# Optimization experiments

Measured on AMD Instinct MI355X. Metric: run time of the kernel, lower is better.

Reference implementation:

```python
import jax, jax.numpy as jnp
import numpy as np

H = 1000   # hidden_size
B = 64     # batch
S = 512    # encoder source length


def setup_inputs() -> dict:
    key = jax.random.key(0)
    ks = jax.random.split(key, 9)
    scale = 0.02
    return {
        "decoder_hidden": jax.random.normal(ks[0], (1, B, H), jnp.float32),
        "context": jax.random.normal(ks[1], (B, S, 2 * H), jnp.float32),
        "mask": jax.random.randint(ks[2], (B, S, 1), 0, 2) == 1,
        "W_a": jax.random.normal(ks[3], (H, 2 * H), jnp.float32) * scale,
        "W_b": jax.random.normal(ks[4], (H, H), jnp.float32) * scale,
        "W_c_w": jax.random.normal(ks[5], (1, H), jnp.float32) * scale,
        "W_c_b": jax.random.normal(ks[6], (1,), jnp.float32) * scale,
        "dense_w": jax.random.normal(ks[7], (H, 2 * H), jnp.float32) * scale,
        "dense_b": jax.random.normal(ks[8], (H,), jnp.float32) * scale,
    }


def reference(decoder_hidden, context, mask, W_a, W_b, W_c_w, W_c_b, dense_w, dense_b):
    # context_in: (B, S, H)
    context_in = jnp.einsum('bsd,hd->bsh', context, W_a)
    # hidden_in: (1, B, H) @ W_b.T -> transpose(0,1) -> (B, 1, H)
    hidden_in = jnp.transpose(jnp.einsum('nbd,hd->nbh', decoder_hidden, W_b), (1, 0, 2))
    # scores: (B, S, 1)
    attention = jnp.einsum('bsh,oh->bso', jnp.tanh(context_in + hidden_in), W_c_w) + W_c_b
    attention = jnp.where(mask, jnp.asarray(-1e6, attention.dtype), attention)
    attention_softmaxed = jax.nn.softmax(attention, axis=1)  # softmax over source length
    # weighted_sum: (B, 1, S) x (B, S, 2H) -> (B, 1, 2H)
    weighted_sum = jnp.einsum('bso,bsd->bod', attention_softmaxed, context)
    # dense: (B, 1, H)
    return jnp.einsum('bod,hd->boh', weighted_sum, dense_w) + dense_b
```

## Files before the change

### kernel.cpp

```cpp
#include <hip/hip_runtime.h>
#include <hip/hip_bf16.h>

#define H 1000
#define B 64
#define S 512
#define D 2000
#define KP 2048
#define NP 1024
#define MP 32768
#define KS 10

typedef __attribute__((ext_vector_type(8))) short short8;
typedef __attribute__((ext_vector_type(4))) float f32x4;
typedef __attribute__((ext_vector_type(16))) float f32x16;

__device__ inline unsigned short f2bf(float f) {
  __hip_bfloat16 h = __float2bfloat16(f);
  union { __hip_bfloat16 h; unsigned short u; } c; c.h = h;
  return c.u;
}
__device__ inline float bf2f(unsigned short u) {
  union { unsigned u; float f; } x; x.u = ((unsigned)u) << 16;
  return x.f;
}
__device__ inline float tanh_fast(float x) {
  float e2 = __expf(2.f * x);
  return 1.f - 2.f / (e2 + 1.f);
}

__global__ __launch_bounds__(256) void k_dect(const float* __restrict__ dec,
                                              float* __restrict__ dec_t) {
  const int d = blockIdx.x * 4 + (threadIdx.x >> 6);
  const int b = threadIdx.x & 63;
  dec_t[d * 64 + b] = dec[b * H + d];
}

__global__ __launch_bounds__(256) void k_hidden2(const float* __restrict__ dec_t,
                                                 const float* __restrict__ Wb,
                                                 float* __restrict__ hi) {
  const int h = blockIdx.x * 4 + (threadIdx.x >> 6);
  const int lane = threadIdx.x & 63;
  const float* w = Wb + (size_t)h * H;
  float acc = 0.f;
#pragma unroll 4
  for (int d = 0; d < H; ++d) acc += w[d] * dec_t[d * 64 + lane];
  hi[lane * H + h] = acc;
}

__global__ __launch_bounds__(256) void k_hidden(const float* __restrict__ dec,
                                                const float* __restrict__ Wb,
                                                float* __restrict__ hi) {
  __shared__ float sdec[H];
  const int b = blockIdx.y;
  const int h = blockIdx.x * 4 + (threadIdx.x >> 6);
  const int lane = threadIdx.x & 63;
  for (int d = threadIdx.x; d < H; d += 256) sdec[d] = dec[b * H + d];
  __syncthreads();
  const float* w = Wb + (size_t)h * H;
  float acc = 0.f;
  for (int d = lane; d < H; d += 64) acc += w[d] * sdec[d];
  for (int o = 32; o; o >>= 1) acc += __shfl_xor(acc, o);
  if (lane == 0) hi[b * H + h] = acc;
}

__global__ __launch_bounds__(256) void k_cvt_t(const float* __restrict__ src,
                                               unsigned short* __restrict__ dst,
                                               int valid_rows) {
  __shared__ unsigned short st[2][8192];
  const int rp = blockIdx.x;
  const int tid = threadIdx.x;
  const int r0 = tid >> 2;
  const int kq = tid & 3;

#define CVT_BODY(T, P)                                                          \
  do {                                                                          \
    const int t = (T);                                                          \
    unsigned short v[4][8];                                                     \
    _Pragma("unroll")                                                           \
    for (int w = 0; w < 4; ++w) {                                               \
      const int grow = rp * 256 + r0 + w * 64;                                  \
      const int gcol = t * 32 + kq * 8;                                         \
      if (grow < valid_rows && gcol + 8 <= D) {                                 \
        const float* p = src + (size_t)grow * D + gcol;                         \
        float4 x = *(const float4*)p;                                           \
        float4 y = *(const float4*)(p + 4);                                     \
        v[w][0] = f2bf(x.x); v[w][1] = f2bf(x.y); v[w][2] = f2bf(x.z);          \
        v[w][3] = f2bf(x.w); v[w][4] = f2bf(y.x); v[w][5] = f2bf(y.y);          \
        v[w][6] = f2bf(y.z); v[w][7] = f2bf(y.w);                               \
      } else {                                                                  \
        _Pragma("unroll")                                                       \
        for (int z = 0; z < 8; ++z) v[w][z] = 0;                                \
      }                                                                         \
    }                                                                           \
    _Pragma("unroll")                                                           \
    for (int w = 0; w < 4; ++w)                                                 \
      *(short8*)&st[P][(kq * 256 + r0 + w * 64) * 8] = *(short8*)&v[w][0];      \
    __syncthreads();                                                            \
    unsigned short* ob = dst + ((size_t)rp * 64 + t) * 8192;                    \
    _Pragma("unroll")                                                           \
    for (int s = 0; s < 4; ++s)                                                 \
      *(short8*)(ob + (tid + s * 256) * 8) = *(short8*)&st[P][(tid + s * 256) * 8]; \
  } while (0)

  const int t0 = blockIdx.y * 8;
  for (int tt = 0; tt < 8; tt += 2) {
    CVT_BODY(t0 + tt, 0);
    CVT_BODY(t0 + tt + 1, 1);
  }
#undef CVT_BODY
}

__global__ __launch_bounds__(512) void k_scores_fast(const unsigned short* __restrict__ ctxb,
                                                     const unsigned short* __restrict__ wab,
                                                     const float* __restrict__ hi,
                                                     const float* __restrict__ Wcw,
                                                     float* __restrict__ scores) {
  __shared__ unsigned short As[3][8192];
  __shared__ unsigned short Bs[3][8192];

  const int bid = blockIdx.x;
  const int swz = (bid & 7) * 64 + (bid >> 3);
  const int rtile = swz >> 2;
  const int ctile = swz & 3;
  const int row0 = rtile * 256;
  const int col0 = ctile * 256;

  const int tid = threadIdx.x;
  const int lane = tid & 63;
  const int wid = tid >> 6;
  const int wm = wid >> 2;
  const int wn = wid & 3;
  const int ln31 = lane & 31;
  const int kh = lane >> 5;

  const unsigned short* ga = ctxb + (size_t)rtile * (64 * 8192);
  const unsigned short* gb = wab + (size_t)ctile * (64 * 8192);

  f32x16 acc[4][2];
#pragma unroll
  for (int i = 0; i < 4; ++i)
#pragma unroll
    for (int j = 0; j < 2; ++j)
#pragma unroll
      for (int r = 0; r < 16; ++r) acc[i][j][r] = 0.f;

#define STAGE(T, BUF)                                                                                      \
  do {                                                                                                     \
    const unsigned short* pa = ga + (size_t)(T) * 8192 + tid * 8;                                          \
    const unsigned short* pb = gb + (size_t)(T) * 8192 + tid * 8;                                          \
    __builtin_amdgcn_global_load_lds((const __attribute__((address_space(1))) unsigned int*)pa,            \
                                     (__attribute__((address_space(3))) unsigned int*)&As[BUF][tid * 8],   \
                                     16, 0, 0);                                                            \
    __builtin_amdgcn_global_load_lds((const __attribute__((address_space(1))) unsigned int*)(pa + 4096),   \
                                     (__attribute__((address_space(3))) unsigned int*)&As[BUF][tid * 8 + 4096], \
                                     16, 0, 0);                                                            \
    __builtin_amdgcn_global_load_lds((const __attribute__((address_space(1))) unsigned int*)pb,            \
                                     (__attribute__((address_space(3))) unsigned int*)&Bs[BUF][tid * 8],   \
                                     16, 0, 0);                                                            \
    __builtin_amdgcn_global_load_lds((const __attribute__((address_space(1))) unsigned int*)(pb + 4096),   \
                                     (__attribute__((address_space(3))) unsigned int*)&Bs[BUF][tid * 8 + 4096], \
                                     16, 0, 0);                                                            \
  } while (0)

  const int abase = kh * 2048 + (wm * 128 + ln31) * 8;
  const int bbase = kh * 2048 + (wn * 64 + ln31) * 8;

#define COMPUTE(BI)                                                                     \
  do {                                                                                  \
    _Pragma("unroll")                                                                   \
    for (int ks = 0; ks < 2; ++ks) {                                                    \
      short8 a[4], bb[2];                                                               \
      _Pragma("unroll")                                                                 \
      for (int mi = 0; mi < 4; ++mi)                                                    \
        a[mi] = *(const short8*)&As[BI][abase + ks * 4096 + mi * 256];                  \
      _Pragma("unroll")                                                                 \
      for (int ni = 0; ni < 2; ++ni)                                                    \
        bb[ni] = *(const short8*)&Bs[BI][bbase + ks * 4096 + ni * 256];                 \
      __builtin_amdgcn_s_setprio(1);                                                    \
      _Pragma("unroll")                                                                 \
      for (int mi = 0; mi < 4; ++mi)                                                    \
        _Pragma("unroll")                                                               \
        for (int ni = 0; ni < 2; ++ni)                                                  \
          acc[mi][ni] = __builtin_amdgcn_mfma_f32_32x32x16_bf16(a[mi], bb[ni], acc[mi][ni], 0, 0, 0); \
      __builtin_amdgcn_s_setprio(0);                                                    \
    }                                                                                   \
  } while (0)

#define ITER(T, BC, BS)                                      \
  do {                                                       \
    STAGE((T) + 2, BS);                                      \
    COMPUTE(BC);                                             \
    asm volatile("s_waitcnt vmcnt(4)" ::: "memory");         \
    __builtin_amdgcn_s_barrier();                            \
  } while (0)

  STAGE(0, 0);
  STAGE(1, 1);
  asm volatile("s_waitcnt vmcnt(4)" ::: "memory");
  __builtin_amdgcn_s_barrier();

  for (int t = 0; t < 60; t += 3) {
    ITER(t, 0, 2);
    ITER(t + 1, 1, 0);
    ITER(t + 2, 2, 1);
  }
  ITER(60, 0, 2);
  ITER(61, 1, 0);
  COMPUTE(2);
  asm volatile("s_waitcnt vmcnt(0)" ::: "memory");
  __builtin_amdgcn_s_barrier();
  COMPUTE(0);
#undef ITER
#undef STAGE
#undef COMPUTE

  const int b_idx = row0 >> 9;
  float wc[2], hv[2];
#pragma unroll
  for (int ni = 0; ni < 2; ++ni) {
    const int h = col0 + wn * 64 + ni * 32 + ln31;
    wc[ni] = (h < H) ? Wcw[h] : 0.f;
    hv[ni] = (h < H) ? hi[b_idx * H + h] : 0.f;
  }
#pragma unroll
  for (int mi = 0; mi < 4; ++mi) {
#pragma unroll
    for (int reg = 0; reg < 16; ++reg) {
      float p = wc[0] * tanh_fast(acc[mi][0][reg] + hv[0])
              + wc[1] * tanh_fast(acc[mi][1][reg] + hv[1]);
      p += __shfl_xor(p, 1);
      p += __shfl_xor(p, 2);
      p += __shfl_xor(p, 4);
      p += __shfl_xor(p, 8);
      p += __shfl_xor(p, 16);
      if (ln31 == 0) {
        const int n = row0 + wm * 128 + mi * 32 + (reg & 3) + 8 * (reg >> 2) + 4 * kh;
        atomicAdd(&scores[n], p);
      }
    }
  }
}

#define BM 128
#define BN 128
#define BK 32
#define NT 63
__global__ __launch_bounds__(256) void k_scores(const float* __restrict__ ctx,
                                                const float* __restrict__ Wa,
                                                const float* __restrict__ hi,
                                                const float* __restrict__ Wcw,
                                                float* __restrict__ scores) {
  __shared__ unsigned short As[2][BM][BK];
  __shared__ unsigned short Bs[2][BN][BK];

  const int bid = blockIdx.x;
  const int swz = (bid & 7) * 256 + (bid >> 3);
  const int row0 = (swz >> 3) * BM;
  const int col0 = (swz & 7) * BN;

  const int tid = threadIdx.x;
  const int lane = tid & 63;
  const int wid = tid >> 6;
  const int wm = wid >> 1;
  const int wn = wid & 1;
  const int fr = lane & 15;
  const int fq = lane >> 4;

  const int trow = tid >> 1;
  const int thalf = tid & 1;

  f32x4 acc[4][4];
#pragma unroll
  for (int i = 0; i < 4; ++i)
#pragma unroll
    for (int j = 0; j < 4; ++j) acc[i][j] = (f32x4){0.f, 0.f, 0.f, 0.f};

  const float* aptr = ctx + (size_t)(row0 + trow) * D + thalf * 16;
  const int hB = col0 + trow;
  const bool bvalid = (hB < H);
  const float* bptr = Wa + (size_t)(bvalid ? hB : 0) * D + thalf * 16;

  float4 ra[4], rb[4];

#define LOADT(T)                                                     \
  do {                                                               \
    const int base = (T) * BK + thalf * 16;                          \
    _Pragma("unroll")                                                \
    for (int q = 0; q < 4; ++q) {                                    \
      const int kk = base + q * 4;                                   \
      if (kk < D) {                                                  \
        ra[q] = *(const float4*)(aptr + (T) * BK + q * 4);           \
        if (bvalid) rb[q] = *(const float4*)(bptr + (T) * BK + q * 4); \
      }                                                              \
    }                                                                \
  } while (0)

#define CVTW(T, BUF)                                                 \
  do {                                                               \
    const int base = (T) * BK + thalf * 16;                          \
    unsigned short ta[16], tb[16];                                   \
    _Pragma("unroll")                                                \
    for (int q = 0; q < 4; ++q) {                                    \
      const int kk = base + q * 4;                                   \
      const bool v = (kk < D);                                       \
      ta[q * 4 + 0] = v ? f2bf(ra[q].x) : 0;                         \
      ta[q * 4 + 1] = v ? f2bf(ra[q].y) : 0;                         \
      ta[q * 4 + 2] = v ? f2bf(ra[q].z) : 0;                         \
      ta[q * 4 + 3] = v ? f2bf(ra[q].w) : 0;                         \
      const bool vb = v && bvalid;                                   \
      tb[q * 4 + 0] = vb ? f2bf(rb[q].x) : 0;                        \
      tb[q * 4 + 1] = vb ? f2bf(rb[q].y) : 0;                        \
      tb[q * 4 + 2] = vb ? f2bf(rb[q].z) : 0;                        \
      tb[q * 4 + 3] = vb ? f2bf(rb[q].w) : 0;                        \
    }                                                                \
    *(short8*)&As[BUF][trow][thalf * 16]     = *(short8*)&ta[0];     \
    *(short8*)&As[BUF][trow][thalf * 16 + 8] = *(short8*)&ta[8];     \
    *(short8*)&Bs[BUF][trow][thalf * 16]     = *(short8*)&tb[0];     \
    *(short8*)&Bs[BUF][trow][thalf * 16 + 8] = *(short8*)&tb[8];     \
  } while (0)

  LOADT(0);
  CVTW(0, 0);
  LOADT(1);
  __syncthreads();

  int cur = 0;
  for (int t = 0; t < NT; ++t) {
    short8 a[4], bbf[4];
#pragma unroll
    for (int mi = 0; mi < 4; ++mi)
      a[mi] = *(const short8*)&As[cur][wm * 64 + mi * 16 + fr][fq * 8];
#pragma unroll
    for (int ni = 0; ni < 4; ++ni)
      bbf[ni] = *(const short8*)&Bs[cur][wn * 64 + ni * 16 + fr][fq * 8];
#pragma unroll
    for (int mi = 0; mi < 4; ++mi)
#pragma unroll
      for (int ni = 0; ni < 4; ++ni)
        acc[mi][ni] = __builtin_amdgcn_mfma_f32_16x16x32_bf16(a[mi], bbf[ni], acc[mi][ni], 0, 0, 0);

    if (t + 1 < NT) {
      CVTW(t + 1, cur ^ 1);
      if (t + 2 < NT) LOADT(t + 2);
    }
    __syncthreads();
    cur ^= 1;
  }
#undef LOADT
#undef CVTW

  const int b_idx = row0 >> 9;
  float wcv[4], hiv[4];
#pragma unroll
  for (int ni = 0; ni < 4; ++ni) {
    const int h = col0 + wn * 64 + ni * 16 + fr;
    wcv[ni] = (h < H) ? Wcw[h] : 0.f;
    hiv[ni] = (h < H) ? hi[b_idx * H + h] : 0.f;
  }
#pragma unroll
  for (int mi = 0; mi < 4; ++mi) {
#pragma unroll
    for (int r = 0; r < 4; ++r) {
      float p = 0.f;
#pragma unroll
      for (int ni = 0; ni < 4; ++ni)
        p += wcv[ni] * tanhf(acc[mi][ni][r] + hiv[ni]);
      p += __shfl_xor(p, 1);
      p += __shfl_xor(p, 2);
      p += __shfl_xor(p, 4);
      p += __shfl_xor(p, 8);
      if (fr == 0)
        atomicAdd(&scores[row0 + wm * 64 + mi * 16 + fq * 4 + r], p);
    }
  }
}

__global__ __launch_bounds__(256) void k_softmax(const float* __restrict__ scores,
                                                 const int* __restrict__ mask,
                                                 const float* __restrict__ Wcb,
                                                 float* __restrict__ probs) {
  __shared__ float buf[S];
  __shared__ float rbuf[256];
  const int b = blockIdx.x;
  const float bias = Wcb[0];
  float mx = -3.4e38f;
  for (int s = threadIdx.x; s < S; s += 256) {
    float a = mask[b * S + s] ? -1e6f : (scores[b * S + s] + bias);
    buf[s] = a;
    mx = fmaxf(mx, a);
  }
  rbuf[threadIdx.x] = mx;
  __syncthreads();
  for (int w = 128; w > 0; w >>= 1) {
    if (threadIdx.x < w) rbuf[threadIdx.x] = fmaxf(rbuf[threadIdx.x], rbuf[threadIdx.x + w]);
    __syncthreads();
  }
  mx = rbuf[0];
  __syncthreads();
  float sum = 0.f;
  for (int s = threadIdx.x; s < S; s += 256) {
    float e = expf(buf[s] - mx);
    buf[s] = e;
    sum += e;
  }
  rbuf[threadIdx.x] = sum;
  __syncthreads();
  for (int w = 128; w > 0; w >>= 1) {
    if (threadIdx.x < w) rbuf[threadIdx.x] += rbuf[threadIdx.x + w];
    __syncthreads();
  }
  const float inv = 1.f / rbuf[0];
  for (int s = threadIdx.x; s < S; s += 256) probs[b * S + s] = buf[s] * inv;
}

__global__ __launch_bounds__(256) void k_wsum_b(const unsigned short* __restrict__ ctxb,
                                                const float* __restrict__ probs,
                                                float* __restrict__ ws2) {
  __shared__ float sp[S];
  const int t = blockIdx.x;
  const int b = blockIdx.y;
  const int tid = threadIdx.x;
  const int p = tid >> 6;
  const int lane = tid & 63;
  for (int i = tid; i < S; i += 256) sp[i] = probs[b * S + i];
  __syncthreads();
  float acc[8];
#pragma unroll
  for (int e = 0; e < 8; ++e) acc[e] = 0.f;
#pragma unroll
  for (int rt = 0; rt < 2; ++rt) {
    const unsigned short* chunk = ctxb + ((size_t)(b * 2 + rt) * 64 + t) * 8192;
#pragma unroll
    for (int half = 0; half < 4; ++half) {
      const int row = half * 64 + lane;
      short8 v = *(const short8*)&chunk[(p * 256 + row) * 8];
      const float pv = sp[rt * 256 + row];
#pragma unroll
      for (int e = 0; e < 8; ++e) acc[e] += pv * bf2f((unsigned short)v[e]);
    }
  }
#pragma unroll
  for (int o = 32; o; o >>= 1)
#pragma unroll
    for (int e = 0; e < 8; ++e) acc[e] += __shfl_xor(acc[e], o);
  const int d0 = t * 32 + p * 8;
  if (lane == 0 && d0 < D) {
#pragma unroll
    for (int e = 0; e < 8; ++e) ws2[(size_t)b * D + d0 + e] = acc[e];
  }
}

__global__ __launch_bounds__(256) void k_wsum(const float* __restrict__ ctx,
                                              const float* __restrict__ probs,
                                              float* __restrict__ ws2) {
  __shared__ float p[S];
  const int b = blockIdx.y;
  const int d = blockIdx.x * 256 + threadIdx.x;
  for (int s = threadIdx.x; s < S; s += 256) p[s] = probs[b * S + s];
  __syncthreads();
  if (d < D) {
    float acc = 0.f;
    for (int s = 0; s < S; ++s) acc += p[s] * ctx[(size_t)(b * S + s) * D + d];
    ws2[b * D + d] = acc;
  }
}

__global__ __launch_bounds__(256) void k_dense_part(const float* __restrict__ ws2,
                                                    const float* __restrict__ Dw,
                                                    float* __restrict__ partial) {
  __shared__ float sw[64][201];
  const int tid = threadIdx.x;
  const int ks = blockIdx.y;
  const int k0 = ks * 200;
  for (int idx = tid; idx < 64 * 200; idx += 256) {
    const int b = idx / 200, k = idx - b * 200;
    sw[b][k] = ws2[(size_t)b * D + k0 + k];
  }
  __syncthreads();
  const int h = blockIdx.x * 4 + (tid >> 6);
  const int lane = tid & 63;
  const float* wrow = Dw + (size_t)h * D + k0;
  float acc = 0.f;
#pragma unroll 8
  for (int k = 0; k < 200; ++k) acc += wrow[k] * sw[lane][k];
  partial[((size_t)ks * 64 + lane) * 1000 + h] = acc;
}

__global__ __launch_bounds__(256) void k_dense_red(const float* __restrict__ partial,
                                                   const float* __restrict__ Db,
                                                   float* __restrict__ out) {
  const int idx = blockIdx.x * 256 + threadIdx.x;
  const int h = idx % 1000;
  float acc = Db[h];
#pragma unroll
  for (int ks = 0; ks < KS; ++ks) acc += partial[(size_t)ks * 64000 + idx];
  out[idx] = acc;
}

__global__ __launch_bounds__(256) void k_dense(const float* __restrict__ ws2,
                                               const float* __restrict__ Dw,
                                               const float* __restrict__ Db,
                                               float* __restrict__ out) {
  __shared__ float v[D];
  const int b = blockIdx.y;
  const int h = blockIdx.x * 256 + threadIdx.x;
  for (int d = threadIdx.x; d < D; d += 256) v[d] = ws2[b * D + d];
  __syncthreads();
  if (h < H) {
    const float* w = Dw + (size_t)h * D;
    float acc = 0.f;
    for (int d = 0; d < D; ++d) acc += w[d] * v[d];
    out[b * H + h] = acc + Db[h];
  }
}

extern "C" void kernel_launch(void* const* d_in, const int* in_sizes, int n_in,
                              void* d_out, int out_size, void* d_ws, size_t ws_size,
                              hipStream_t stream) {
  const float* dec = (const float*)d_in[0];
  const float* ctx = (const float*)d_in[1];
  const int*   mask = (const int*)d_in[2];
  const float* Wa  = (const float*)d_in[3];
  const float* Wb  = (const float*)d_in[4];
  const float* Wcw = (const float*)d_in[5];
  const float* Wcb = (const float*)d_in[6];
  const float* Dw  = (const float*)d_in[7];
  const float* Db  = (const float*)d_in[8];
  float* out = (float*)d_out;

  float* hi     = (float*)d_ws;
  float* scores = hi + B * H;
  float* probs  = scores + B * S;
  float* ws2    = probs + B * S;
  const size_t float_words = (size_t)B * H + 2 * B * S + B * D;
  unsigned short* ctx_b = (unsigned short*)((float*)d_ws + float_words);
  unsigned short* wa_b  = ctx_b + (size_t)MP * KP;
  float* dec_t  = (float*)ctx_b;
  float* partial = (float*)ctx_b;
  const size_t need = float_words * 4 + ((size_t)MP * KP + (size_t)NP * KP) * 2;

  hipMemsetAsync(scores, 0, B * S * sizeof(float), stream);
  if (ws_size >= need) {
    k_dect<<<250, 256, 0, stream>>>(dec, dec_t);
    k_hidden2<<<250, 256, 0, stream>>>(dec_t, Wb, hi);
    k_cvt_t<<<dim3(MP / 256, 8), 256, 0, stream>>>(ctx, ctx_b, MP);
    k_cvt_t<<<dim3(NP / 256, 8), 256, 0, stream>>>(Wa, wa_b, H);
    k_scores_fast<<<512, 512, 0, stream>>>(ctx_b, wa_b, hi, Wcw, scores);
    k_softmax<<<B, 256, 0, stream>>>(scores, mask, Wcb, probs);
    k_wsum_b<<<dim3(63, B), 256, 0, stream>>>(ctx_b, probs, ws2);
    k_dense_part<<<dim3(250, KS), 256, 0, stream>>>(ws2, Dw, partial);
    k_dense_red<<<250, 256, 0, stream>>>(partial, Db, out);
  } else {
    k_hidden<<<dim3(250, B), 256, 0, stream>>>(dec, Wb, hi);
    k_scores<<<2048, 256, 0, stream>>>(ctx, Wa, hi, Wcw, scores);
    k_softmax<<<B, 256, 0, stream>>>(scores, mask, Wcb, probs);
    k_wsum<<<dim3((D + 255) / 256, B), 256, 0, stream>>>(ctx, probs, ws2);
    k_dense<<<dim3((H + 255) / 256, B), 256, 0, stream>>>(ws2, Dw, Db, out);
  }
}
```

Baseline: 408.5 us.

## Double scores GEMM block threads and fuse softmax into weighted-sum kernel

The scores GEMM now launches 1024 threads per block, 16 waves each owning a 64x64 sub-tile instead of 8 waves with 128x64. Each thread issues half as many LDS-direct loads, and the waitcnt values drop to match. The softmax kernel is removed: every weighted-sum block recomputes the masked softmax for its batch row from the raw scores before accumulating. This cuts a launch and the probs round trip, at the cost of redundant softmax work across 63 blocks per batch row and a possible change in GEMM occupancy and register pressure.

Result: no change. 407.4 us (-0.3%).

```diff
diff --git a/kernel.cpp b/kernel.cpp
--- a/kernel.cpp
+++ b/kernel.cpp
@@ -110,11 +110,11 @@
 #undef CVT_BODY
 }
 
-__global__ __launch_bounds__(512) void k_scores_fast(const unsigned short* __restrict__ ctxb,
-                                                     const unsigned short* __restrict__ wab,
-                                                     const float* __restrict__ hi,
-                                                     const float* __restrict__ Wcw,
-                                                     float* __restrict__ scores) {
+__global__ __launch_bounds__(1024) void k_scores_fast(const unsigned short* __restrict__ ctxb,
+                                                      const unsigned short* __restrict__ wab,
+                                                      const float* __restrict__ hi,
+                                                      const float* __restrict__ Wcw,
+                                                      float* __restrict__ scores) {
   __shared__ unsigned short As[3][8192];
   __shared__ unsigned short Bs[3][8192];
 
@@ -136,9 +136,9 @@
   const unsigned short* ga = ctxb + (size_t)rtile * (64 * 8192);
   const unsigned short* gb = wab + (size_t)ctile * (64 * 8192);
 
-  f32x16 acc[4][2];
-#pragma unroll
-  for (int i = 0; i < 4; ++i)
+  f32x16 acc[2][2];
+#pragma unroll
+  for (int i = 0; i < 2; ++i)
 #pragma unroll
     for (int j = 0; j < 2; ++j)
 #pragma unroll
@@ -151,34 +151,28 @@
     __builtin_amdgcn_global_load_lds((const __attribute__((address_space(1))) unsigned int*)pa,            \
                                      (__attribute__((address_space(3))) unsigned int*)&As[BUF][tid * 8],   \
                                      16, 0, 0);                                                            \
-    __builtin_amdgcn_global_load_lds((const __attribute__((address_space(1))) unsigned int*)(pa + 4096),   \
-                                     (__attribute__((address_space(3))) unsigned int*)&As[BUF][tid * 8 + 4096], \
-                                     16, 0, 0);                                                            \
     __builtin_amdgcn_global_load_lds((const __attribute__((address_space(1))) unsigned int*)pb,            \
                                      (__attribute__((address_space(3))) unsigned int*)&Bs[BUF][tid * 8],   \
                                      16, 0, 0);                                                            \
-    __builtin_amdgcn_global_load_lds((const __attribute__((address_space(1))) unsigned int*)(pb + 4096),   \
-                                     (__attribute__((address_space(3))) unsigned int*)&Bs[BUF][tid * 8 + 4096], \
-                                     16, 0, 0);                                                            \
   } while (0)
 
-  const int abase = kh * 2048 + (wm * 128 + ln31) * 8;
+  const int abase = kh * 2048 + (wm * 64 + ln31) * 8;
   const int bbase = kh * 2048 + (wn * 64 + ln31) * 8;
 
 #define COMPUTE(BI)                                                                     \
   do {                                                                                  \
     _Pragma("unroll")                                                                   \
     for (int ks = 0; ks < 2; ++ks) {                                                    \
-      short8 a[4], bb[2];                                                               \
+      short8 a[2], bb[2];                                                               \
       _Pragma("unroll")                                                                 \
-      for (int mi = 0; mi < 4; ++mi)                                                    \
+      for (int mi = 0; mi < 2; ++mi)                                                    \
         a[mi] = *(const short8*)&As[BI][abase + ks * 4096 + mi * 256];                  \
       _Pragma("unroll")                                                                 \
       for (int ni = 0; ni < 2; ++ni)                                                    \
         bb[ni] = *(const short8*)&Bs[BI][bbase + ks * 4096 + ni * 256];                 \
       __builtin_amdgcn_s_setprio(1);                                                    \
       _Pragma("unroll")                                                                 \
-      for (int mi = 0; mi < 4; ++mi)                                                    \
+      for (int mi = 0; mi < 2; ++mi)                                                    \
         _Pragma("unroll")                                                               \
         for (int ni = 0; ni < 2; ++ni)                                                  \
           acc[mi][ni] = __builtin_amdgcn_mfma_f32_32x32x16_bf16(a[mi], bb[ni], acc[mi][ni], 0, 0, 0); \
@@ -190,13 +184,13 @@
   do {                                                       \
     STAGE((T) + 2, BS);                                      \
     COMPUTE(BC);                                             \
-    asm volatile("s_waitcnt vmcnt(4)" ::: "memory");         \
+    asm volatile("s_waitcnt vmcnt(2)" ::: "memory");         \
     __builtin_amdgcn_s_barrier();                            \
   } while (0)
 
   STAGE(0, 0);
   STAGE(1, 1);
-  asm volatile("s_waitcnt vmcnt(4)" ::: "memory");
+  asm volatile("s_waitcnt vmcnt(2)" ::: "memory");
   __builtin_amdgcn_s_barrier();
 
   for (int t = 0; t < 60; t += 3) {
@@ -223,7 +217,7 @@
     hv[ni] = (h < H) ? hi[b_idx * H + h] : 0.f;
   }
 #pragma unroll
-  for (int mi = 0; mi < 4; ++mi) {
+  for (int mi = 0; mi < 2; ++mi) {
 #pragma unroll
     for (int reg = 0; reg < 16; ++reg) {
       float p = wc[0] * tanh_fast(acc[mi][0][reg] + hv[0])
@@ -234,7 +228,7 @@
       p += __shfl_xor(p, 8);
       p += __shfl_xor(p, 16);
       if (ln31 == 0) {
-        const int n = row0 + wm * 128 + mi * 32 + (reg & 3) + 8 * (reg >> 2) + 4 * kh;
+        const int n = row0 + wm * 64 + mi * 32 + (reg & 3) + 8 * (reg >> 2) + 4 * kh;
         atomicAdd(&scores[n], p);
       }
     }
@@ -413,17 +407,39 @@
   for (int s = threadIdx.x; s < S; s += 256) probs[b * S + s] = buf[s] * inv;
 }
 
-__global__ __launch_bounds__(256) void k_wsum_b(const unsigned short* __restrict__ ctxb,
-                                                const float* __restrict__ probs,
-                                                float* __restrict__ ws2) {
+__global__ __launch_bounds__(256) void k_wsum_sm(const unsigned short* __restrict__ ctxb,
+                                                 const float* __restrict__ scores,
+                                                 const int* __restrict__ mask,
+                                                 const float* __restrict__ Wcb,
+                                                 float* __restrict__ ws2) {
   __shared__ float sp[S];
+  __shared__ float red[8];
   const int t = blockIdx.x;
   const int b = blockIdx.y;
   const int tid = threadIdx.x;
   const int p = tid >> 6;
   const int lane = tid & 63;
-  for (int i = tid; i < S; i += 256) sp[i] = probs[b * S + i];
-  __syncthreads();
+  const float bias = Wcb[0];
+
+  float a0 = mask[b * S + tid] ? -1e6f : (scores[b * S + tid] + bias);
+  float a1 = mask[b * S + tid + 256] ? -1e6f : (scores[b * S + tid + 256] + bias);
+  float m = fmaxf(a0, a1);
+#pragma unroll
+  for (int o = 32; o; o >>= 1) m = fmaxf(m, __shfl_xor(m, o));
+  if (lane == 0) red[p] = m;
+  __syncthreads();
+  m = fmaxf(fmaxf(red[0], red[1]), fmaxf(red[2], red[3]));
+  float e0 = expf(a0 - m), e1 = expf(a1 - m);
+  float s = e0 + e1;
+#pragma unroll
+  for (int o = 32; o; o >>= 1) s += __shfl_xor(s, o);
+  if (lane == 0) red[4 + p] = s;
+  __syncthreads();
+  const float inv = 1.f / (red[4] + red[5] + red[6] + red[7]);
+  sp[tid] = e0 * inv;
+  sp[tid + 256] = e1 * inv;
+  __syncthreads();
+
   float acc[8];
 #pragma unroll
   for (int e = 0; e < 8; ++e) acc[e] = 0.f;
@@ -545,9 +561,8 @@
     k_hidden2<<<250, 256, 0, stream>>>(dec_t, Wb, hi);
     k_cvt_t<<<dim3(MP / 256, 8), 256, 0, stream>>>(ctx, ctx_b, MP);
     k_cvt_t<<<dim3(NP / 256, 8), 256, 0, stream>>>(Wa, wa_b, H);
-    k_scores_fast<<<512, 512, 0, stream>>>(ctx_b, wa_b, hi, Wcw, scores);
-    k_softmax<<<B, 256, 0, stream>>>(scores, mask, Wcb, probs);
-    k_wsum_b<<<dim3(63, B), 256, 0, stream>>>(ctx_b, probs, ws2);
+    k_scores_fast<<<512, 1024, 0, stream>>>(ctx_b, wa_b, hi, Wcw, scores);
+    k_wsum_sm<<<dim3(63, B), 256, 0, stream>>>(ctx_b, scores, mask, Wcb, ws2);
     k_dense_part<<<dim3(250, KS), 256, 0, stream>>>(ws2, Dw, partial);
     k_dense_red<<<250, 256, 0, stream>>>(partial, Db, out);
   } else {
```
